# Optimization experiments

Measured on AMD Instinct MI355X. Metric: run time of the kernel, lower is better.

Reference implementation:

```python
import jax, jax.numpy as jnp
import numpy as np
import math

RCR = 5.2
RCA = 3.5
NUM_SPECIES = 4


def _triu_index(num_species):
    s1, s2 = np.triu_indices(num_species)
    ret = np.zeros((num_species, num_species), dtype=np.int32)
    ret[s1, s2] = np.arange(len(s1))
    ret[s2, s1] = np.arange(len(s1))
    return ret


def _cutoff_cosine(d, rc):
    return 0.5 * jnp.cos(d * (math.pi / rc)) + 0.5


def setup_inputs():
    key = jax.random.key(0)
    k1, k2 = jax.random.split(key)
    M, A = 32, 48
    BOX = 8.0  # ~0.43 atoms/A^3, realistic organic density
    coordinates = jax.random.uniform(k1, (M, A, 3), dtype=jnp.float32) * BOX
    species = jax.random.randint(k2, (M, A), 0, NUM_SPECIES)
    EtaR = jnp.array([16.0], dtype=jnp.float32)
    ShfR = jnp.asarray(0.9 + (RCR - 0.9) / 16.0 * np.arange(16), dtype=jnp.float32)
    EtaA = jnp.array([8.0], dtype=jnp.float32)
    Zeta = jnp.array([32.0], dtype=jnp.float32)
    ShfA = jnp.asarray(0.9 + (RCA - 0.9) / 4.0 * np.arange(4), dtype=jnp.float32)
    ShfZ = jnp.asarray((np.arange(8) + 0.5) * np.pi / 8.0, dtype=jnp.float32)
    return {"coordinates": coordinates, "EtaR": EtaR, "ShfR": ShfR,
            "EtaA": EtaA, "Zeta": Zeta, "ShfA": ShfA, "ShfZ": ShfZ,
            "species": species}


def _compute_aev(coordinates, EtaR, ShfR, EtaA, Zeta, ShfA, ShfZ, species):
    M, A, _ = coordinates.shape
    S = NUM_SPECIES
    npairs_sp = S * (S + 1) // 2  # 10 unordered species pairs
    rad_sub = EtaR.shape[0] * ShfR.shape[0]   # 16
    ang_sub = EtaA.shape[0] * Zeta.shape[0] * ShfA.shape[0] * ShfZ.shape[0]  # 32

    diff = coordinates[:, :, None, :] - coordinates[:, None, :, :]  # (M,A,A,3)
    D = jnp.linalg.norm(diff, axis=-1)                              # (M,A,A)
    mrow = jnp.arange(M)[:, None]

    # ---------- radial AEV (eq. 3) ----------
    p1, p2 = np.triu_indices(A, 1)                                  # static (P,)
    d = D[:, p1, p2]                                                # (M,P)
    mask_r = (d <= RCR).astype(d.dtype)
    du = d[:, :, None, None]                                        # (M,P,1,1)
    fc = _cutoff_cosine(du, RCR)
    rt = 0.25 * jnp.exp(-EtaR[:, None] * (du - ShfR[None, :]) ** 2) * fc
    rt = (rt * mask_r[:, :, None, None]).reshape(M, len(p1), rad_sub)
    sp = species
    idx1 = p1[None, :] * S + sp[:, p2]                              # (M,P)
    idx2 = p2[None, :] * S + sp[:, p1]
    radial = jnp.zeros((M, A * S, rad_sub), dtype=rt.dtype)
    radial = radial.at[mrow, idx1].add(rt).at[mrow, idx2].add(rt)
    radial = radial.reshape(M, A, S * rad_sub)

    # ---------- angular AEV (eq. 4) ----------
    # static triple list: central atom i with unordered neighbor pair (j,k), j,k != i
    jj, kk = np.triu_indices(A - 1, 1)
    tri = []
    for i in range(A):
        others = np.concatenate([np.arange(i), np.arange(i + 1, A)])
        tri.append(np.stack([np.full(jj.shape, i), others[jj], others[kk]], 1))
    tri = np.concatenate(tri)                                       # (T,3)
    ci, n1, n2 = tri[:, 0], tri[:, 1], tri[:, 2]

    v1 = coordinates[:, n1] - coordinates[:, ci]                    # (M,T,3)
    v2 = coordinates[:, n2] - coordinates[:, ci]
    d1 = D[:, ci, n1]
    d2 = D[:, ci, n2]
    mask_a = ((d1 <= RCA) & (d2 <= RCA)).astype(d1.dtype)           # (M,T)
    eps = 1e-8  # torch cosine_similarity eps
    cos = 0.95 * jnp.sum(v1 * v2, -1) / (jnp.maximum(d1, eps) * jnp.maximum(d2, eps))
    ang = jnp.arccos(cos)                                           # (M,T)

    # broadcast axes: (M, T, EtaA, Zeta, ShfA, ShfZ) as in torchani constants
    EtaA_b = EtaA.reshape(1, 1, -1, 1, 1, 1)
    Zeta_b = Zeta.reshape(1, 1, 1, -1, 1, 1)
    ShfA_b = ShfA.reshape(1, 1, 1, 1, -1, 1)
    ShfZ_b = ShfZ.reshape(1, 1, 1, 1, 1, -1)
    a6 = ang[:, :, None, None, None, None]
    dm = ((d1 + d2) / 2)[:, :, None, None, None, None]
    fcj = (_cutoff_cosine(d1, RCA) * _cutoff_cosine(d2, RCA))[:, :, None, None, None, None]
    f1 = ((1 + jnp.cos(a6 - ShfZ_b)) / 2) ** Zeta_b
    f2 = jnp.exp(-EtaA_b * (dm - ShfA_b) ** 2)
    at = (2 * f1 * f2 * fcj).reshape(M, tri.shape[0], ang_sub)
    at = at * mask_a[:, :, None]

    triu = jnp.asarray(_triu_index(S))
    pidx = triu[sp[:, n1], sp[:, n2]]                               # (M,T)
    flat = ci[None, :] * npairs_sp + pidx
    angular = jnp.zeros((M, A * npairs_sp, ang_sub), dtype=at.dtype)
    angular = angular.at[mrow, flat].add(at).reshape(M, A, npairs_sp * ang_sub)

    return jnp.concatenate([radial, angular], axis=-1)              # (M,A,384)


def reference(coordinates, EtaR, ShfR, EtaA, Zeta, ShfA, ShfZ, species):
    return _compute_aev(coordinates, EtaR, ShfR, EtaA, Zeta, ShfA, ShfZ, species)
```

## Files before the change

kernel.cpp:

```cpp
#include <hip/hip_runtime.h>
#include <hip/hip_bf16.h>


#define NA 48
#define RCR_F 5.2f
#define RCA_F 3.5f
#define PI_F 3.14159265358979f
#define LOG2E_F 1.44269504088896f
#define RADLEN 64
#define AEVLEN 384

struct Smem {
    float sx[NA], sy[NA], sz[NA];
    int   ssp[NA];
    float ra[NA]; unsigned rbu[NA];
    float ad[NA], avx[NA], avy[NA], avz[NA], afc[NA]; int asp[NA];
    int   nR, nAn;
    float rpart[4][64];
    float apart[4][320];
};

template <typename T> __device__ __forceinline__ float toF(const T* p, int i);
template <> __device__ __forceinline__ float toF<float>(const float* p, int i) { return p[i]; }
template <> __device__ __forceinline__ float toF<__hip_bfloat16>(const __hip_bfloat16* p, int i) { return __bfloat162float(p[i]); }

template <typename T> __device__ __forceinline__ void stF(T* p, size_t i, float v);
template <> __device__ __forceinline__ void stF<float>(float* p, size_t i, float v) { p[i] = v; }
template <> __device__ __forceinline__ void stF<__hip_bfloat16>(__hip_bfloat16* p, size_t i, float v) { p[i] = __float2bfloat16(v); }

__device__ __forceinline__ int triu_idx(int a, int b) {
    int lo = a < b ? a : b;
    int hi = a < b ? b : a;
    return lo * 4 - (lo * (lo - 1)) / 2 + (hi - lo);
}

template <typename T>
__device__ void aev_body(Smem& sm,
    const T* __restrict__ coords, const T* __restrict__ etaR_p,
    const T* __restrict__ shfR_p, const T* __restrict__ etaA_p,
    const T* __restrict__ zeta_p, const T* __restrict__ shfA_p,
    const T* __restrict__ shfZ_p, const int* __restrict__ species,
    T* __restrict__ out)
{
    const int tid  = threadIdx.x;
    const int lane = tid & 63;
    const int w    = tid >> 6;
    const int bid  = blockIdx.x;
    const int m  = bid / NA;
    const int ci = bid % NA;

    const float etaR = toF(etaR_p, 0);
    const float etaA = toF(etaA_p, 0);
    const float zeta = toF(zeta_p, 0);
    const float kR   = etaR * LOG2E_F;
    const float k2   = etaA * LOG2E_F;

    if (tid < NA) {
        int g = m * NA + tid;
        sm.sx[tid]  = toF(coords, 3 * g + 0);
        sm.sy[tid]  = toF(coords, 3 * g + 1);
        sm.sz[tid]  = toF(coords, 3 * g + 2);
        sm.ssp[tid] = species[g];
    }
    __syncthreads();

    if (w == 0) {
        const float cx = sm.sx[ci], cy = sm.sy[ci], cz = sm.sz[ci];
        float dx = 0.f, dy = 0.f, dz = 0.f, d = 1e30f;
        if (lane < NA && lane != ci) {
            dx = sm.sx[lane] - cx; dy = sm.sy[lane] - cy; dz = sm.sz[lane] - cz;
            d = sqrtf(dx * dx + dy * dy + dz * dz);
        }
        unsigned long long mR = __ballot(d <= RCR_F);
        unsigned long long mA = __ballot(d <= RCA_F);
        unsigned long long lanebit = 1ull << lane;
        unsigned long long below = lanebit - 1ull;
        if (mR & lanebit) {
            int s = __popcll(mR & below);
            float fcR = 0.5f * __cosf(d * (PI_F / RCR_F)) + 0.5f;
            float rb = fmaxf(__log2f(0.25f * fcR) - kR * d * d, -8.0e4f);
            sm.ra[s]  = 2.f * kR * d;
            sm.rbu[s] = (__float_as_uint(rb) & ~3u) | (unsigned)sm.ssp[lane];
        }
        if (mA & lanebit) {
            int s = __popcll(mA & below);
            sm.ad[s]  = d;
            sm.avx[s] = dx; sm.avy[s] = dy; sm.avz[s] = dz;
            sm.afc[s] = 0.5f * __cosf(d * (PI_F / RCA_F)) + 0.5f;
            sm.asp[s] = sm.ssp[lane];
        }
        if (lane == 0) { sm.nR = (int)__popcll(mR); sm.nAn = (int)__popcll(mA); }
    }
    __syncthreads();

    const int nR  = sm.nR;
    const int nAn = sm.nAn;

    const float myShfR = toF(shfR_p, lane & 15);
    const int   mySp   = lane >> 4;
    const int   myA    = (lane >> 3) & 3;
    const float myShfA = toF(shfA_p, myA);
    const float myShfZ = toF(shfZ_p, lane & 7);
    const float myCz = __cosf(myShfZ);
    const float mySz = __sinf(myShfZ);
    const int   p0   = lane >> 5;
    const bool  isLo = (p0 == 0);
    const bool  z32  = (zeta == 32.f);
    const float myLc = k2 * myShfA * myShfA;
    const float myRc = kR * myShfR * myShfR;

    float racc = 0.f;
    for (int i = w; i < nR; i += 4) {
        unsigned ru = sm.rbu[i];
        float arg = __builtin_fmaf(sm.ra[i], myShfR, __uint_as_float(ru)) - myRc;
        float t = __builtin_amdgcn_exp2f(arg);
        racc += ((int)(ru & 3u) == mySp) ? t : 0.f;
    }
    sm.rpart[w][lane] = racc;

    float a0 = 0.f, a1 = 0.f, a2 = 0.f, a3 = 0.f, a4 = 0.f;
    const int np = nAn * (nAn - 1) / 2;
    const int cnt_w = (np > w) ? ((np - w + 3) >> 2) : 0;
    for (int base = 0; base < cnt_w; base += 64) {
        int i = base + lane;
        int p = 4 * i + w;
        int pp = (i < cnt_w) ? p : 0;
        int j = 0, rem = pp, span = nAn - 1;
        while (rem >= span) { rem -= span; span--; j++; }
        int k = j + 1 + rem;
        float d1 = sm.ad[j], d2 = sm.ad[k];
        float dot = sm.avx[j] * sm.avx[k] + sm.avy[j] * sm.avy[k] + sm.avz[j] * sm.avz[k];
        float cv = 0.95f * dot / (fmaxf(d1, 1e-8f) * (fmaxf(d2, 1e-8f)));
        float sv = sqrtf(fmaxf(1.f - cv * cv, 0.f));
        float dm = 0.5f * (d1 + d2);
        float fc2 = 2.f * sm.afc[j] * sm.afc[k];
        float pe = fmaxf(-k2 * dm * dm + __log2f(fc2), -8.0e4f);
        float pd = 2.f * k2 * dm;
        unsigned int pu = (__float_as_uint(pe) & ~15u) | (unsigned)triu_idx(sm.asp[j], sm.asp[k]);

        int cnt = cnt_w - base; if (cnt > 64) cnt = 64;
        for (int q = 0; q < cnt; q++) {
            float qc = __shfl(cv, q);
            float qs = __shfl(sv, q);
            float qd = __shfl(pd, q);
            unsigned int qu = (unsigned)__shfl((int)pu, q);
            float qpe = __uint_as_float(qu);
            float cd = qc * myCz + qs * mySz;
            float x = 0.5f + 0.5f * cd;
            float f1;
            if (z32) { float x2 = x*x, x4 = x2*x2, x8 = x4*x4, x16 = x8*x8; f1 = x16*x16; }
            else     { f1 = __powf(x, zeta); }
            float term = f1 * __builtin_amdgcn_exp2f(qd * myShfA + qpe - myLc);
            int qp = __builtin_amdgcn_readfirstlane((int)(qu & 15u));
            switch (qp) {
                case 0: a0 += isLo ? term : 0.f; break;
                case 1: a0 += isLo ? 0.f : term; break;
                case 2: a1 += isLo ? term : 0.f; break;
                case 3: a1 += isLo ? 0.f : term; break;
                case 4: a2 += isLo ? term : 0.f; break;
                case 5: a2 += isLo ? 0.f : term; break;
                case 6: a3 += isLo ? term : 0.f; break;
                case 7: a3 += isLo ? 0.f : term; break;
                case 8: a4 += isLo ? term : 0.f; break;
                case 9: a4 += isLo ? 0.f : term; break;
            }
        }
    }
    sm.apart[w][lane + 0]   = a0;
    sm.apart[w][lane + 64]  = a1;
    sm.apart[w][lane + 128] = a2;
    sm.apart[w][lane + 192] = a3;
    sm.apart[w][lane + 256] = a4;
    __syncthreads();

    const size_t ob = (size_t)bid * AEVLEN;
    if (tid < 64) {
        float r = sm.rpart[0][tid] + sm.rpart[1][tid] + sm.rpart[2][tid] + sm.rpart[3][tid];
        stF(out, ob + tid, r);
    }
    {
        float v = sm.apart[0][tid] + sm.apart[1][tid] + sm.apart[2][tid] + sm.apart[3][tid];
        stF(out, ob + RADLEN + tid, v);
    }
    if (tid < 64) {
        int s = 256 + tid;
        float v = sm.apart[0][s] + sm.apart[1][s] + sm.apart[2][s] + sm.apart[3][s];
        stF(out, ob + RADLEN + s, v);
    }
}

__global__ __launch_bounds__(256) void aev_kernel(
    const void* coords, const void* etaR, const void* shfR, const void* etaA,
    const void* zeta, const void* shfA, const void* shfZ,
    const int* __restrict__ species, void* out)
{
    __shared__ Smem sm;
    const float probe = __uint_as_float(((const unsigned int*)shfR)[0]);
    if (probe > 0.85f && probe < 0.95f) {
        aev_body<float>(sm, (const float*)coords, (const float*)etaR,
                        (const float*)shfR, (const float*)etaA, (const float*)zeta,
                        (const float*)shfA, (const float*)shfZ, species, (float*)out);
    } else {
        aev_body<__hip_bfloat16>(sm, (const __hip_bfloat16*)coords,
                        (const __hip_bfloat16*)etaR, (const __hip_bfloat16*)shfR,
                        (const __hip_bfloat16*)etaA, (const __hip_bfloat16*)zeta,
                        (const __hip_bfloat16*)shfA, (const __hip_bfloat16*)shfZ,
                        species, (__hip_bfloat16*)out);
    }
}

extern "C" void kernel_launch(void* const* d_in, const int* in_sizes, int n_in,
                              void* d_out, int out_size, void* d_ws, size_t ws_size,
                              hipStream_t stream) {
    aev_kernel<<<dim3(32 * NA), dim3(256), 0, stream>>>(
        d_in[0], d_in[1], d_in[2], d_in[3], d_in[4], d_in[5], d_in[6],
        (const int*)d_in[7], d_out);
}
```

Baseline: 81.41 us.

## Assign one angular pair per lane and accumulate via LDS atomics

Before, each wave broadcast every angular pair to all 64 lanes, and each lane computed one of the 64 (pair-species-half, sub-feature) outputs. Now each lane handles a whole triplet pair and computes all 32 angular sub-features itself, adding them into a padded (stride 33) per-wave shared buffer with atomicAdd. The pair index is now found with a closed-form sqrt instead of a loop. This removes the serial shuffle loop, the readfirstlane switch and the wasted work on the inactive half. In exchange it adds up to 32 LDS atomics per pair, which may conflict when lanes hit the same species pair, and uses more registers.

```diff
diff --git a/kernel.cpp b/kernel.cpp
--- a/kernel.cpp
+++ b/kernel.cpp
@@ -17,7 +17,7 @@
     float ad[NA], avx[NA], avy[NA], avz[NA], afc[NA]; int asp[NA];
     int   nR, nAn;
     float rpart[4][64];
-    float apart[4][320];
+    float apart[4][330];
 };
 
 template <typename T> __device__ __forceinline__ float toF(const T* p, int i);
@@ -62,6 +62,7 @@
         sm.sz[tid]  = toF(coords, 3 * g + 2);
         sm.ssp[tid] = species[g];
     }
+    for (int i = lane; i < 330; i += 64) sm.apart[w][i] = 0.f;
     __syncthreads();
 
     if (w == 0) {
@@ -98,16 +99,8 @@
 
     const float myShfR = toF(shfR_p, lane & 15);
     const int   mySp   = lane >> 4;
-    const int   myA    = (lane >> 3) & 3;
-    const float myShfA = toF(shfA_p, myA);
-    const float myShfZ = toF(shfZ_p, lane & 7);
-    const float myCz = __cosf(myShfZ);
-    const float mySz = __sinf(myShfZ);
-    const int   p0   = lane >> 5;
-    const bool  isLo = (p0 == 0);
-    const bool  z32  = (zeta == 32.f);
-    const float myLc = k2 * myShfA * myShfA;
-    const float myRc = kR * myShfR * myShfR;
+    const float myRc   = kR * myShfR * myShfR;
+    const bool  z32    = (zeta == 32.f);
 
     float racc = 0.f;
     for (int i = w; i < nR; i += 4) {
@@ -118,59 +111,53 @@
     }
     sm.rpart[w][lane] = racc;
 
-    float a0 = 0.f, a1 = 0.f, a2 = 0.f, a3 = 0.f, a4 = 0.f;
+    float czv[8], szv[8], shfa[4], lca[4];
+    #pragma unroll
+    for (int z = 0; z < 8; z++) {
+        float s = toF(shfZ_p, z);
+        czv[z] = __cosf(s);
+        szv[z] = __sinf(s);
+    }
+    #pragma unroll
+    for (int a = 0; a < 4; a++) {
+        shfa[a] = toF(shfA_p, a);
+        lca[a]  = k2 * shfa[a] * shfa[a];
+    }
+
     const int np = nAn * (nAn - 1) / 2;
-    const int cnt_w = (np > w) ? ((np - w + 3) >> 2) : 0;
-    for (int base = 0; base < cnt_w; base += 64) {
-        int i = base + lane;
-        int p = 4 * i + w;
-        int pp = (i < cnt_w) ? p : 0;
-        int j = 0, rem = pp, span = nAn - 1;
-        while (rem >= span) { rem -= span; span--; j++; }
-        int k = j + 1 + rem;
+    for (int p = 4 * lane + w; p < np; p += 256) {
+        const int b = 2 * nAn - 1;
+        float s = sqrtf((float)(b * b - 8 * p));
+        int j = (int)(((float)b - s) * 0.5f);
+        if ((j + 1) * (b - 1 - j) <= 2 * p) j++;
+        if (j * (b - j) > 2 * p) j--;
+        int k = p - ((j * (b - j)) >> 1) + j + 1;
+
         float d1 = sm.ad[j], d2 = sm.ad[k];
         float dot = sm.avx[j] * sm.avx[k] + sm.avy[j] * sm.avy[k] + sm.avz[j] * sm.avz[k];
-        float cv = 0.95f * dot / (fmaxf(d1, 1e-8f) * (fmaxf(d2, 1e-8f)));
+        float cv = 0.95f * dot / (fmaxf(d1, 1e-8f) * fmaxf(d2, 1e-8f));
         float sv = sqrtf(fmaxf(1.f - cv * cv, 0.f));
         float dm = 0.5f * (d1 + d2);
         float fc2 = 2.f * sm.afc[j] * sm.afc[k];
         float pe = fmaxf(-k2 * dm * dm + __log2f(fc2), -8.0e4f);
         float pd = 2.f * k2 * dm;
-        unsigned int pu = (__float_as_uint(pe) & ~15u) | (unsigned)triu_idx(sm.asp[j], sm.asp[k]);
-
-        int cnt = cnt_w - base; if (cnt > 64) cnt = 64;
-        for (int q = 0; q < cnt; q++) {
-            float qc = __shfl(cv, q);
-            float qs = __shfl(sv, q);
-            float qd = __shfl(pd, q);
-            unsigned int qu = (unsigned)__shfl((int)pu, q);
-            float qpe = __uint_as_float(qu);
-            float cd = qc * myCz + qs * mySz;
-            float x = 0.5f + 0.5f * cd;
+        float peA0 = pe - lca[0], peA1 = pe - lca[1];
+        float peA2 = pe - lca[2], peA3 = pe - lca[3];
+        float* dst = &sm.apart[w][triu_idx(sm.asp[j], sm.asp[k]) * 33];
+
+        #pragma unroll
+        for (int z = 0; z < 8; z++) {
+            float cd = __builtin_fmaf(cv, czv[z], sv * szv[z]);
+            float x = __builtin_fmaf(0.5f, cd, 0.5f);
             float f1;
             if (z32) { float x2 = x*x, x4 = x2*x2, x8 = x4*x4, x16 = x8*x8; f1 = x16*x16; }
             else     { f1 = __powf(x, zeta); }
-            float term = f1 * __builtin_amdgcn_exp2f(qd * myShfA + qpe - myLc);
-            int qp = __builtin_amdgcn_readfirstlane((int)(qu & 15u));
-            switch (qp) {
-                case 0: a0 += isLo ? term : 0.f; break;
-                case 1: a0 += isLo ? 0.f : term; break;
-                case 2: a1 += isLo ? term : 0.f; break;
-                case 3: a1 += isLo ? 0.f : term; break;
-                case 4: a2 += isLo ? term : 0.f; break;
-                case 5: a2 += isLo ? 0.f : term; break;
-                case 6: a3 += isLo ? term : 0.f; break;
-                case 7: a3 += isLo ? 0.f : term; break;
-                case 8: a4 += isLo ? term : 0.f; break;
-                case 9: a4 += isLo ? 0.f : term; break;
-            }
-        }
-    }
-    sm.apart[w][lane + 0]   = a0;
-    sm.apart[w][lane + 64]  = a1;
-    sm.apart[w][lane + 128] = a2;
-    sm.apart[w][lane + 192] = a3;
-    sm.apart[w][lane + 256] = a4;
+            atomicAdd(dst +  0 + z, f1 * __builtin_amdgcn_exp2f(__builtin_fmaf(pd, shfa[0], peA0)));
+            atomicAdd(dst +  8 + z, f1 * __builtin_amdgcn_exp2f(__builtin_fmaf(pd, shfa[1], peA1)));
+            atomicAdd(dst + 16 + z, f1 * __builtin_amdgcn_exp2f(__builtin_fmaf(pd, shfa[2], peA2)));
+            atomicAdd(dst + 24 + z, f1 * __builtin_amdgcn_exp2f(__builtin_fmaf(pd, shfa[3], peA3)));
+        }
+    }
     __syncthreads();
 
     const size_t ob = (size_t)bid * AEVLEN;
@@ -179,13 +166,17 @@
         stF(out, ob + tid, r);
     }
     {
-        float v = sm.apart[0][tid] + sm.apart[1][tid] + sm.apart[2][tid] + sm.apart[3][tid];
-        stF(out, ob + RADLEN + tid, v);
+        int row = tid >> 5, f = tid & 31;
+        int s = row * 33 + f;
+        float v = sm.apart[0][s] + sm.apart[1][s] + sm.apart[2][s] + sm.apart[3][s];
+        stF(out, ob + RADLEN + row * 32 + f, v);
     }
     if (tid < 64) {
-        int s = 256 + tid;
+        int idx = 256 + tid;
+        int row = idx >> 5, f = idx & 31;
+        int s = row * 33 + f;
         float v = sm.apart[0][s] + sm.apart[1][s] + sm.apart[2][s] + sm.apart[3][s];
-        stF(out, ob + RADLEN + s, v);
+        stF(out, ob + RADLEN + row * 32 + f, v);
     }
 }
 
```

After: 101.0 us. +24.1%, slower.
